# Performance work log

Hardware: AMD Instinct MI355X
Metric: run time of the kernel (lower is better)

## Reference

```python
import jax, jax.numpy as jnp
import numpy as np

WIN = 7
K1 = 0.01
K2 = 0.03
COV_NORM = WIN * WIN / (WIN * WIN - 1.0)  # unbiased covariance correction


def _box_filter(t):
    # t: [B, 1, H, W]; valid conv with uniform 7x7 window (mean filter)
    w = jnp.ones((1, 1, WIN, WIN), t.dtype) / (WIN * WIN)
    return jax.lax.conv_general_dilated(
        t, w, window_strides=(1, 1), padding='VALID',
        dimension_numbers=('NCHW', 'OIHW', 'NCHW'))


def setup_inputs() -> dict:
    key = jax.random.key(0)
    kx, ky = jax.random.split(key)
    B, C, H, W = 64, 1, 384, 384
    X = jax.random.normal(kx, (B, C, H, W), dtype=jnp.float32)
    Y = jax.random.normal(ky, (B, C, H, W), dtype=jnp.float32)
    data_range = jnp.ones((B,), dtype=jnp.float32)
    return {"X": X, "Y": Y, "data_range": data_range}


def reference(X, Y, data_range):
    ux = _box_filter(X)
    uy = _box_filter(Y)
    uxx = _box_filter(X * X)
    uxy = _box_filter(X * Y)
    uyy = _box_filter(Y * Y)

    vx = COV_NORM * (uxx - ux * ux)
    vy = COV_NORM * (uyy - uy * uy)
    vxy = COV_NORM * (uxy - ux * uy)

    L = data_range.reshape(-1, 1, 1, 1)  # per-sample dynamic range
    C1 = (K1 * L) ** 2
    C2 = (K2 * L) ** 2

    N1 = 2.0 * ux * uy + C1
    N2 = 2.0 * vxy + C2
    D1 = ux * ux + uy * uy + C1
    D2 = vx + vy + C2
    S = (N1 * N2) / (D1 * D2)

    # original: mean SSIM per sample, then mean over batch; equal-size maps so
    # this equals the mean over the per-sample means
    per_sample = jnp.mean(S, axis=(1, 2, 3))
    return 1.0 - jnp.mean(per_sample)
```

## Files before the change

kernel.cpp:

```cpp
#include <hip/hip_runtime.h>

#define IMH 384
#define IMW 384
#define OH 378
#define OW 378
#define NB 64
#define SROWS 18
#define INROWS 24
#define NSTRIP 21
#define BLOCK 256
#define GSTRIDE 26
#define NPAIR 12
#define SLOTF 384
#define NBLK (NSTRIP * NB)


template <int CTRL>
__device__ __forceinline__ float dpp_sh(float v) {
    return __int_as_float(__builtin_amdgcn_update_dpp(
        0, __float_as_int(v), CTRL, 0xf, 0xf, true));
}

__device__ __forceinline__ float2 f2add(float2 a, float2 b) { return make_float2(a.x + b.x, a.y + b.y); }
__device__ __forceinline__ float2 f2sub(float2 a, float2 b) { return make_float2(a.x - b.x, a.y - b.y); }
__device__ __forceinline__ float2 f2mul(float2 a, float2 b) { return make_float2(a.x * b.x, a.y * b.y); }
__device__ __forceinline__ float2 f2fma(float2 a, float2 b, float2 c) {
    return make_float2(fmaf(a.x, b.x, c.x), fmaf(a.y, b.y, c.y));
}
__device__ __forceinline__ float2 f2fnma(float2 a, float2 b, float2 c) {
    return make_float2(fmaf(-a.x, b.x, c.x), fmaf(-a.y, b.y, c.y));
}
__device__ __forceinline__ float2 f2fms(float2 a, float s, float2 c) {
    return make_float2(fmaf(a.x, s, -c.x), fmaf(a.y, s, -c.y));
}
__device__ __forceinline__ float2 f2s(float s) { return make_float2(s, s); }

__device__ __forceinline__ void stage16(const float* g, float* l) {
    __builtin_amdgcn_global_load_lds(
        (const __attribute__((address_space(1))) uint32_t*)(g),
        (__attribute__((address_space(3))) uint32_t*)(l),
        16, 0, 0);
}

#define WAITV(n) asm volatile("s_waitcnt vmcnt(" #n ")" ::: "memory")
#define RAWBAR() asm volatile("s_barrier" ::: "memory")

__global__ __launch_bounds__(BLOCK)
__attribute__((amdgpu_waves_per_eu(6, 6)))
void ssim_kernel(
    const float* __restrict__ X, const float* __restrict__ Y,
    const float* __restrict__ data_range, float* __restrict__ partials)
{
    const int tid   = threadIdx.x;
    const int g     = tid >> 4;
    const int j     = tid & 15;
    const int strip = blockIdx.x;
    const int b     = blockIdx.y;
    const int y0    = strip * SROWS;

    __shared__ float sX[4][2][SLOTF];
    __shared__ float sY[4][2][SLOTF];

    const int wv   = tid >> 6;
    const int ln   = tid & 63;
    const bool isX = (wv < 2);
    const int half = wv & 1;
    const int foff = half * 128 + ln * 4;
    const float* __restrict__ gstg =
        (isX ? X : Y) + b * (IMH * IMW) + y0 * IMW + foff;
    float* const lbase = (isX ? &sX[0][0][0] : &sY[0][0][0]) + half * 128;

    const int ce  = g * GSTRIDE + 2 * j;
    const int cin = min(ce, IMW - 2);
    const float2 vmask = make_float2(
        ((j <= 12) && (ce     < OW)) ? 1.f : 0.f,
        ((j <= 12) && (ce + 1 < OW)) ? 1.f : 0.f);

    const float L   = data_range[b];
    const float c1s = (0.49f * L) * (0.49f * L);
    const float c2s = (1.47f * L) * (1.47f * L);
    const float k1  = 49.0f / 48.0f;
    const float k2  = 49.0f / 24.0f;
    asm volatile("" :: "v"(c1s), "v"(c2s));
    __builtin_amdgcn_sched_barrier(0);

    #pragma unroll
    for (int q = 0; q < 4; ++q) {
        stage16(gstg + (2 * q) * IMW,     lbase + (2 * q + 0) * SLOTF);
        stage16(gstg + (2 * q + 1) * IMW, lbase + (2 * q + 1) * SLOTF);
    }
    WAITV(6);
    RAWBAR();
    float2 cx0 = *(const float2*)&sX[0][0][cin];
    float2 cx1 = *(const float2*)&sX[0][1][cin];
    float2 cy0 = *(const float2*)&sY[0][0][cin];
    float2 cy1 = *(const float2*)&sY[0][1][cin];

    float2 xh[7], yh[7];
    #pragma unroll
    for (int k = 0; k < 7; ++k) { xh[k] = f2s(0.f); yh[k] = f2s(0.f); }
    float2 V0 = f2s(0.f), V1 = f2s(0.f), V2 = f2s(0.f),
           V3 = f2s(0.f), V4 = f2s(0.f);
    float2 ls2 = f2s(0.f);

    auto rowcompute = [&](int r, float2 x, float2 y) {
        const int ks = r % 7;
        const float2 xo = xh[ks], yo = yh[ks];
        V0 = f2add(V0, f2sub(x, xo));
        V1 = f2add(V1, f2sub(y, yo));
        V2 = f2fma(x, x, V2);  V2 = f2fnma(xo, xo, V2);
        V3 = f2fma(x, y, V3);  V3 = f2fnma(xo, yo, V3);
        V4 = f2fma(y, y, V4);  V4 = f2fnma(yo, yo, V4);
        xh[ks] = x; yh[ks] = y;

        if (r >= 6) {
            const float2 V24 = f2add(V2, V4);
            const float2 Vv[4] = {V0, V1, V24, V3};
            float Se[4], So[4];
            #pragma unroll
            for (int q = 0; q < 4; ++q) {
                const float e  = Vv[q].x;
                const float o  = Vv[q].y;
                const float pp = e + o;
                float B = pp + dpp_sh<0x101>(pp);
                float C = B + dpp_sh<0x102>(B);
                Se[q] = C - dpp_sh<0x103>(o);
                So[q] = C - e;
            }
            const float2 S0  = make_float2(Se[0], So[0]);
            const float2 S1  = make_float2(Se[1], So[1]);
            const float2 S24 = make_float2(Se[2], So[2]);
            const float2 S3  = make_float2(Se[3], So[3]);

            float2 P  = f2mul(S0, S1);
            float2 q1 = f2mul(S1, S1);
            float2 QQ = f2fma(S0, S0, q1);
            float2 N1 = f2fma(f2s(2.f), P, f2s(c1s));
            float2 D1 = f2add(QQ, f2s(c1s));
            float2 w  = f2fms(S3, 49.0f, P);
            float2 N2 = f2fma(f2s(k2), w, f2s(c2s));
            float2 u  = f2fms(S24, 49.0f, QQ);
            float2 D2 = f2fma(f2s(k1), u, f2s(c2s));
            float2 num = f2mul(N1, N2);
            float2 den = f2mul(D1, D2);
            const float rdd = __builtin_amdgcn_rcpf(den.x * den.y);
            float2 s2 = make_float2(num.x * den.y * rdd,
                                    num.y * den.x * rdd);
            ls2 = f2fma(s2, vmask, ls2);
        }
    };

    static_assert(INROWS == 24 && NPAIR == 12, "ladder");

    #pragma unroll
    for (int p = 1; p < NPAIR; ++p) {
        if      (p <= 9)  WAITV(4);
        else if (p == 10) WAITV(2);
        else              WAITV(0);
        RAWBAR();

        const int sl = p & 3;
        float2 nx0 = *(const float2*)&sX[sl][0][cin];
        float2 nx1 = *(const float2*)&sX[sl][1][cin];
        float2 ny0 = *(const float2*)&sY[sl][0][cin];
        float2 ny1 = *(const float2*)&sY[sl][1][cin];

        rowcompute(2 * (p - 1),     cx0, cy0);
        rowcompute(2 * (p - 1) + 1, cx1, cy1);

        if (p + 3 < NPAIR) {
            const int q = p + 3;
            stage16(gstg + (2 * q) * IMW,     lbase + ((q & 3) * 2 + 0) * SLOTF);
            stage16(gstg + (2 * q + 1) * IMW, lbase + ((q & 3) * 2 + 1) * SLOTF);
        }

        cx0 = nx0; cx1 = nx1; cy0 = ny0; cy1 = ny1;
    }

    rowcompute(22, cx0, cy0);
    rowcompute(23, cx1, cy1);

    float lsum = ls2.x + ls2.y;
    #pragma unroll
    for (int off = 32; off > 0; off >>= 1)
        lsum += __shfl_down(lsum, off, 64);
    __syncthreads();
    if ((tid & 63) == 0) sX[0][0][tid >> 6] = lsum;
    __syncthreads();
    if (tid == 0) {
        partials[b * NSTRIP + strip] =
            sX[0][0][0] + sX[0][0][1] + sX[0][0][2] + sX[0][0][3];
    }
}

__global__ void finalize_kernel(const float* __restrict__ partials,
                                float* __restrict__ out)
{
    float v = 0.f;
    #pragma unroll
    for (int k = 0; k < NBLK / 64; ++k)
        v += partials[threadIdx.x + 64 * k];
    #pragma unroll
    for (int off = 32; off > 0; off >>= 1)
        v += __shfl_down(v, off, 64);
    if (threadIdx.x == 0)
        out[0] = 1.0f - v * (1.0f / (float)(NB * OH * OW));
}

extern "C" void kernel_launch(void* const* d_in, const int* in_sizes, int n_in,
                              void* d_out, int out_size, void* d_ws, size_t ws_size,
                              hipStream_t stream) {
    const float* X  = (const float*)d_in[0];
    const float* Y  = (const float*)d_in[1];
    const float* dr = (const float*)d_in[2];
    float* out = (float*)d_out;
    float* partials = (float*)d_ws;

    dim3 grid(NSTRIP, NB);
    dim3 block(BLOCK);
    ssim_kernel<<<grid, block, 0, stream>>>(X, Y, dr, partials);
    finalize_kernel<<<1, 64, 0, stream>>>(partials, out);
}
```

Measured before the change: 26.58 us.

## Halve strip height and stage whole strip into LDS upfront

Cuts each block's strip from 18 to 9 output rows, doubling the grid to 42 strips per image. All 16 staging rows (15 needed plus one padding row) are now issued to LDS at the start instead of through a 4-slot rotating ring, and the code waits progressively on vmcnt. The aim is more blocks in flight and more loads outstanding per block, to better hide memory latency. The cost is more halo re-reads (15 input rows per 9 outputs instead of 24 per 18), a larger LDS footprint, and a waves-per-eu hint lowered from 6 to 4.

```diff
diff --git a/kernel.cpp b/kernel.cpp
--- a/kernel.cpp
+++ b/kernel.cpp
@@ -5,12 +5,12 @@
 #define OH 378
 #define OW 378
 #define NB 64
-#define SROWS 18
-#define INROWS 24
-#define NSTRIP 21
+#define SROWS 9
+#define INROWS 15
+#define STROWS 16
+#define NSTRIP 42
 #define BLOCK 256
 #define GSTRIDE 26
-#define NPAIR 12
 #define SLOTF 384
 #define NBLK (NSTRIP * NB)
 
@@ -46,7 +46,7 @@
 #define RAWBAR() asm volatile("s_barrier" ::: "memory")
 
 __global__ __launch_bounds__(BLOCK)
-__attribute__((amdgpu_waves_per_eu(6, 6)))
+__attribute__((amdgpu_waves_per_eu(4, 4)))
 void ssim_kernel(
     const float* __restrict__ X, const float* __restrict__ Y,
     const float* __restrict__ data_range, float* __restrict__ partials)
@@ -58,8 +58,8 @@
     const int b     = blockIdx.y;
     const int y0    = strip * SROWS;
 
-    __shared__ float sX[4][2][SLOTF];
-    __shared__ float sY[4][2][SLOTF];
+    __shared__ float sX[STROWS][SLOTF];
+    __shared__ float sY[STROWS][SLOTF];
 
     const int wv   = tid >> 6;
     const int ln   = tid & 63;
@@ -68,7 +68,9 @@
     const int foff = half * 128 + ln * 4;
     const float* __restrict__ gstg =
         (isX ? X : Y) + b * (IMH * IMW) + y0 * IMW + foff;
-    float* const lbase = (isX ? &sX[0][0][0] : &sY[0][0][0]) + half * 128;
+    const float* __restrict__ gstg15 =
+        (isX ? X : Y) + b * (IMH * IMW) + min(y0 + 15, IMH - 1) * IMW + foff;
+    float* const lbase = (isX ? &sX[0][0] : &sY[0][0]) + half * 128;
 
     const int ce  = g * GSTRIDE + 2 * j;
     const int cin = min(ce, IMW - 2);
@@ -85,16 +87,9 @@
     __builtin_amdgcn_sched_barrier(0);
 
     #pragma unroll
-    for (int q = 0; q < 4; ++q) {
-        stage16(gstg + (2 * q) * IMW,     lbase + (2 * q + 0) * SLOTF);
-        stage16(gstg + (2 * q + 1) * IMW, lbase + (2 * q + 1) * SLOTF);
-    }
-    WAITV(6);
-    RAWBAR();
-    float2 cx0 = *(const float2*)&sX[0][0][cin];
-    float2 cx1 = *(const float2*)&sX[0][1][cin];
-    float2 cy0 = *(const float2*)&sY[0][0][cin];
-    float2 cy1 = *(const float2*)&sY[0][1][cin];
+    for (int r = 0; r < STROWS - 1; ++r)
+        stage16(gstg + r * IMW, lbase + r * SLOTF);
+    stage16(gstg15, lbase + (STROWS - 1) * SLOTF);
 
     float2 xh[7], yh[7];
     #pragma unroll
@@ -150,46 +145,40 @@
         }
     };
 
-    static_assert(INROWS == 24 && NPAIR == 12, "ladder");
-
-    #pragma unroll
-    for (int p = 1; p < NPAIR; ++p) {
-        if      (p <= 9)  WAITV(4);
-        else if (p == 10) WAITV(2);
-        else              WAITV(0);
+    static_assert(INROWS == 15 && STROWS == 16, "ladder");
+
+    #pragma unroll
+    for (int p = 0; p < 8; ++p) {
+        if      (p == 0) WAITV(14);
+        else if (p == 1) WAITV(12);
+        else if (p == 2) WAITV(10);
+        else if (p == 3) WAITV(8);
+        else if (p == 4) WAITV(6);
+        else if (p == 5) WAITV(4);
+        else if (p == 6) WAITV(2);
+        else             WAITV(0);
         RAWBAR();
 
-        const int sl = p & 3;
-        float2 nx0 = *(const float2*)&sX[sl][0][cin];
-        float2 nx1 = *(const float2*)&sX[sl][1][cin];
-        float2 ny0 = *(const float2*)&sY[sl][0][cin];
-        float2 ny1 = *(const float2*)&sY[sl][1][cin];
-
-        rowcompute(2 * (p - 1),     cx0, cy0);
-        rowcompute(2 * (p - 1) + 1, cx1, cy1);
-
-        if (p + 3 < NPAIR) {
-            const int q = p + 3;
-            stage16(gstg + (2 * q) * IMW,     lbase + ((q & 3) * 2 + 0) * SLOTF);
-            stage16(gstg + (2 * q + 1) * IMW, lbase + ((q & 3) * 2 + 1) * SLOTF);
+        const float2 x0 = *(const float2*)&sX[2 * p][cin];
+        const float2 y0v = *(const float2*)&sY[2 * p][cin];
+        rowcompute(2 * p, x0, y0v);
+        if (p < 7) {
+            const float2 x1 = *(const float2*)&sX[2 * p + 1][cin];
+            const float2 y1 = *(const float2*)&sY[2 * p + 1][cin];
+            rowcompute(2 * p + 1, x1, y1);
         }
-
-        cx0 = nx0; cx1 = nx1; cy0 = ny0; cy1 = ny1;
     }
-
-    rowcompute(22, cx0, cy0);
-    rowcompute(23, cx1, cy1);
 
     float lsum = ls2.x + ls2.y;
     #pragma unroll
     for (int off = 32; off > 0; off >>= 1)
         lsum += __shfl_down(lsum, off, 64);
     __syncthreads();
-    if ((tid & 63) == 0) sX[0][0][tid >> 6] = lsum;
+    if ((tid & 63) == 0) sX[0][tid >> 6] = lsum;
     __syncthreads();
     if (tid == 0) {
         partials[b * NSTRIP + strip] =
-            sX[0][0][0] + sX[0][0][1] + sX[0][0][2] + sX[0][0][3];
+            sX[0][0] + sX[0][1] + sX[0][2] + sX[0][3];
     }
 }
 
```

New measurement: 28.24 us. 6.3% more time.
